# Optimization experiments

Measured on AMD Instinct MI355X. Metric: run time of the kernel, lower is better.

## Reference

```python
import jax, jax.numpy as jnp
import numpy as np

B, T, V = 32, 100, 20000
E, H, M, DD = 128, 128, 64, 2


def setup_inputs() -> dict:
    key = jax.random.key(0)
    ks = jax.random.split(key, 12)
    x = jax.random.uniform(ks[0], (B, T, V), dtype=jnp.float32)
    # zero out trailing timesteps per example so Masking layer matters
    lens = jax.random.randint(ks[1], (B,), T * 3 // 4, T + 1)
    tmask = (jnp.arange(T)[None, :] < lens[:, None]).astype(jnp.float32)
    x = x * tmask[:, :, None]
    a = jax.random.uniform(ks[2], (B, V), dtype=jnp.float32)
    d = jax.random.normal(ks[3], (B, DD), dtype=jnp.float32)
    # parameters
    emb = jax.random.uniform(ks[4], (V, E), minval=-0.1, maxval=0.1, dtype=jnp.float32)
    s = 1.0 / np.sqrt(E)
    gru_k = jax.random.uniform(ks[5], (E, 3 * H), minval=-s, maxval=s, dtype=jnp.float32)
    gru_rk = jax.random.normal(ks[6], (H, 3 * H), dtype=jnp.float32) / np.sqrt(H)
    gru_b_i = jnp.zeros((3 * H,), jnp.float32)   # input bias (reset_after=True)
    gru_b_r = jnp.zeros((3 * H,), jnp.float32)   # recurrent bias
    s1 = 1.0 / np.sqrt(H + E)
    W1 = jax.random.uniform(ks[7], (H + E, M), minval=-s1, maxval=s1, dtype=jnp.float32)
    b1 = jnp.zeros((M,), jnp.float32)
    s2 = 1.0 / np.sqrt(M + DD)
    W2 = jax.random.uniform(ks[8], (M + DD, 1), minval=-s2, maxval=s2, dtype=jnp.float32)
    b2 = jnp.zeros((1,), jnp.float32)
    return dict(x=x, a=a, d=d, emb=emb, gru_k=gru_k, gru_rk=gru_rk,
                gru_b_i=gru_b_i, gru_b_r=gru_b_r, W1=W1, b1=b1, W2=W2, b2=b2)


def _gru_final_state(xe, mask, gru_k, gru_rk, gru_b_i, gru_b_r):
    # xe: [B,T,E], mask: [B,T] bool. Keras GRU, reset_after=True, eval mode (dropout off).
    Hn = gru_rk.shape[0]
    x_proj = jnp.einsum('bte,eh->bth', xe, gru_k) + gru_b_i  # [B,T,3H]

    def step(h, inp):
        xp_t, m_t = inp                      # [B,3H], [B]
        rec = h @ gru_rk + gru_b_r           # [B,3H]
        xz, xr, xh = jnp.split(xp_t, 3, axis=-1)
        rz, rr, rh = jnp.split(rec, 3, axis=-1)
        z = jax.nn.sigmoid(xz + rz)
        r = jax.nn.sigmoid(xr + rr)
        hh = jnp.tanh(xh + r * rh)
        h_new = z * h + (1.0 - z) * hh
        h = jnp.where(m_t[:, None], h_new, h)  # masked steps carry state
        return h, None

    h0 = jnp.zeros((xe.shape[0], Hn), xe.dtype)
    h_final, _ = jax.lax.scan(step, h0, (jnp.swapaxes(x_proj, 0, 1), jnp.swapaxes(mask, 0, 1)))
    return h_final


def reference(x, a, d, emb, gru_k, gru_rk, gru_b_i, gru_b_r, W1, b1, W2, b2):
    ae = jnp.tanh(a @ emb)                       # [B,E]
    xe = jnp.tanh(jnp.einsum('btv,ve->bte', x, emb))  # [B,T,E]
    mask = jnp.any(xe != 0.0, axis=-1)           # Masking(mask_value=0.0)
    h = _gru_final_state(xe, mask, gru_k, gru_rk, gru_b_i, gru_b_r)  # [B,H]
    c = jnp.tanh(jnp.concatenate([h, ae], axis=1) @ W1 + b1)         # [B,M]
    out = jax.nn.sigmoid(jnp.concatenate([c, d], axis=1) @ W2 + b2)  # [B,1]
    return out
```

## Files before the change

kernel.cpp:

```cpp
#include <hip/hip_runtime.h>

typedef __attribute__((ext_vector_type(8))) short short8;
typedef __attribute__((ext_vector_type(4))) float float4v;

#define V_ 20000

__device__ __forceinline__ unsigned short f2bf(float f) {
    union { float f; unsigned int u; } v; v.f = f;
    unsigned int u = v.u;
    u += 0x7fffu + ((u >> 16) & 1u);
    return (unsigned short)(u >> 16);
}

__device__ __forceinline__ float fast_tanh(float x) {
    float xc = fminf(15.f, fmaxf(-15.f, x));
    float e = __expf(2.f * xc);
    return (e - 1.f) / (e + 1.f);
}

__device__ __forceinline__ float sigmoidf_(float x) {
    float xc = fminf(30.f, fmaxf(-30.f, x));
    return 1.f / (1.f + __expf(-xc));
}

#define GLL16(gp, lp) __builtin_amdgcn_global_load_lds( \
    (const __attribute__((address_space(1))) void*)(gp), \
    (__attribute__((address_space(3))) void*)(lp), 16, 0, 0)

__global__ __launch_bounds__(256) void cvt_embT(const float* __restrict__ emb,
                                                unsigned short* __restrict__ embT) {
    __shared__ unsigned short tile[128 * 65];
    int tid = threadIdx.x;
    int k0 = blockIdx.x * 64;
    const float4v* e4 = (const float4v*)emb;
    #pragma unroll
    for (int c = 0; c < 8; ++c) {
        int l4 = c * 256 + tid;
        int k = l4 >> 5;
        int n4 = l4 & 31;
        float4v f = {0.f, 0.f, 0.f, 0.f};
        if (k0 + k < V_) f = e4[(size_t)(k0 + k) * 32 + n4];
        tile[(n4 * 4 + 0) * 65 + k] = f2bf(f.x);
        tile[(n4 * 4 + 1) * 65 + k] = f2bf(f.y);
        tile[(n4 * 4 + 2) * 65 + k] = f2bf(f.z);
        tile[(n4 * 4 + 3) * 65 + k] = f2bf(f.w);
    }
    __syncthreads();
    #pragma unroll
    for (int c = 0; c < 4; ++c) {
        int l8 = c * 256 + tid;
        int n = l8 >> 3, seg = l8 & 7;
        int kk = k0 + seg * 8;
        if (kk < V_) {
            short8 v;
            #pragma unroll
            for (int i = 0; i < 8; ++i) v[i] = (short)tile[n * 65 + seg * 8 + i];
            *(short8*)(embT + (size_t)n * V_ + kk) = v;
        }
    }
}

__global__ __launch_bounds__(256, 4) void big_gemm(const float* __restrict__ x,
                                                   const float* __restrict__ a,
                                                   const unsigned short* __restrict__ embT,
                                                   float* __restrict__ partial,
                                                   int ks) {
    __shared__ unsigned short Alds[2][128 * 40];
    __shared__ unsigned short Blds[2][128 * 32];
    int tid = threadIdx.x;
    int bx = blockIdx.x, by = blockIdx.y;
    int m0 = bx * 128;
    int per = 625 / ks, extra = 625 % ks;
    int kb0 = by * per + (by < extra ? by : extra);
    int nkb = per + (by < extra ? 1 : 0);

    int lane = tid & 63, wave = tid >> 6;
    int wr = wave >> 1, wc = wave & 1;
    int ln = lane & 15, quad = lane >> 4;

    float4v acc[4][4];
    #pragma unroll
    for (int i = 0; i < 4; ++i)
        #pragma unroll
        for (int j = 0; j < 4; ++j) acc[i][j] = (float4v){0.f, 0.f, 0.f, 0.f};

    int row = tid >> 1, seg = tid & 1;
    int rg = m0 + row;
    int aidx = rg - 3200; aidx = aidx < 0 ? 0 : (aidx > 31 ? 31 : aidx);
    const float* __restrict__ srcA = (rg < 3200) ? (x + (size_t)rg * V_)
                                                 : (a + (size_t)aidx * V_);
    int brow0 = tid >> 2, bkq = tid & 3;
    int wbase = tid & ~63;
    const unsigned short* gB0 = embT + (size_t)brow0 * V_ + bkq * 8;
    const unsigned short* gB1 = embT + (size_t)(64 + brow0) * V_ + bkq * 8;

    float4v fa0, fa1, fa2, fa3;

    {
        int k0 = kb0 * 32;
        const float4v* ap = (const float4v*)(srcA + k0 + seg * 16);
        fa0 = ap[0]; fa1 = ap[1]; fa2 = ap[2]; fa3 = ap[3];
        GLL16(gB0 + k0, &Blds[0][(size_t)wbase * 8]);
        GLL16(gB1 + k0, &Blds[0][(size_t)(256 + wbase) * 8]);
        short8 w0, w1;
        w0[0]=(short)f2bf(fa0.x); w0[1]=(short)f2bf(fa0.y); w0[2]=(short)f2bf(fa0.z); w0[3]=(short)f2bf(fa0.w);
        w0[4]=(short)f2bf(fa1.x); w0[5]=(short)f2bf(fa1.y); w0[6]=(short)f2bf(fa1.z); w0[7]=(short)f2bf(fa1.w);
        w1[0]=(short)f2bf(fa2.x); w1[1]=(short)f2bf(fa2.y); w1[2]=(short)f2bf(fa2.z); w1[3]=(short)f2bf(fa2.w);
        w1[4]=(short)f2bf(fa3.x); w1[5]=(short)f2bf(fa3.y); w1[6]=(short)f2bf(fa3.z); w1[7]=(short)f2bf(fa3.w);
        *(short8*)&Alds[0][row * 40 + seg * 16]     = w0;
        *(short8*)&Alds[0][row * 40 + seg * 16 + 8] = w1;
    }
    __syncthreads();

    for (int it = 0; it < nkb; ++it) {
        int buf = it & 1, nxt = buf ^ 1;
        bool more = (it + 1 < nkb);
        if (more) {
            int k0 = (kb0 + it + 1) * 32;
            const float4v* ap = (const float4v*)(srcA + k0 + seg * 16);
            fa0 = ap[0]; fa1 = ap[1]; fa2 = ap[2]; fa3 = ap[3];
            GLL16(gB0 + k0, &Blds[nxt][(size_t)wbase * 8]);
            GLL16(gB1 + k0, &Blds[nxt][(size_t)(256 + wbase) * 8]);
        }
        short8 af[4];
        #pragma unroll
        for (int i = 0; i < 4; ++i)
            af[i] = *(const short8*)&Alds[buf][(wr * 64 + i * 16 + ln) * 40 + quad * 8];
        #pragma unroll
        for (int j = 0; j < 4; ++j) {
            short8 bf = *(const short8*)&Blds[buf][(wc * 64 + j * 16 + ln) * 32 + quad * 8];
            #pragma unroll
            for (int i = 0; i < 4; ++i)
                acc[i][j] = __builtin_amdgcn_mfma_f32_16x16x32_bf16(af[i], bf, acc[i][j], 0, 0, 0);
        }
        if (more) {
            short8 w0, w1;
            w0[0]=(short)f2bf(fa0.x); w0[1]=(short)f2bf(fa0.y); w0[2]=(short)f2bf(fa0.z); w0[3]=(short)f2bf(fa0.w);
            w0[4]=(short)f2bf(fa1.x); w0[5]=(short)f2bf(fa1.y); w0[6]=(short)f2bf(fa1.z); w0[7]=(short)f2bf(fa1.w);
            w1[0]=(short)f2bf(fa2.x); w1[1]=(short)f2bf(fa2.y); w1[2]=(short)f2bf(fa2.z); w1[3]=(short)f2bf(fa2.w);
            w1[4]=(short)f2bf(fa3.x); w1[5]=(short)f2bf(fa3.y); w1[6]=(short)f2bf(fa3.z); w1[7]=(short)f2bf(fa3.w);
            *(short8*)&Alds[nxt][row * 40 + seg * 16]     = w0;
            *(short8*)&Alds[nxt][row * 40 + seg * 16 + 8] = w1;
        }
        __syncthreads();
    }

    float* dst = partial + (size_t)by * 3328 * 128;
    #pragma unroll
    for (int i = 0; i < 4; ++i) {
        #pragma unroll
        for (int j = 0; j < 4; ++j) {
            int rowb = m0 + wr * 64 + i * 16 + quad * 4;
            int col = wc * 64 + j * 16 + ln;
            #pragma unroll
            for (int r = 0; r < 4; ++r)
                dst[(size_t)(rowb + r) * 128 + col] = acc[i][j][r];
        }
    }
}

__global__ __launch_bounds__(128) void reduce_tanh(const float* __restrict__ partial,
                                                   float* __restrict__ xe,
                                                   float* __restrict__ ae,
                                                   float* __restrict__ maskg,
                                                   int ks) {
    int row = blockIdx.x;
    int e = threadIdx.x;
    float s = 0.f;
    for (int k = 0; k < ks; ++k)
        s += partial[((size_t)k * 3328 + row) * 128 + e];
    float v = fast_tanh(s);
    if (row < 3200) {
        xe[(size_t)row * 128 + e] = v;
        __shared__ int any;
        if (e == 0) any = 0;
        __syncthreads();
        if (v != 0.f) any = 1;
        __syncthreads();
        if (e == 0) maskg[row] = any ? 1.f : 0.f;
    } else {
        ae[(row - 3200) * 128 + e] = v;
    }
}

__global__ __launch_bounds__(384) void xproj_kernel(const float* __restrict__ xe,
                                                    const float* __restrict__ gru_k,
                                                    const float* __restrict__ b_i,
                                                    float* __restrict__ xproj) {
    __shared__ float xs[16 * 128];
    int tid = threadIdx.x;
    int row0 = blockIdx.x * 16;
    const float4v* src = (const float4v*)(xe + (size_t)row0 * 128);
    float4v* dstl = (float4v*)xs;
    #pragma unroll
    for (int c = 0; c < 2; ++c) {
        int i4 = c * 384 + tid;
        if (i4 < 512) dstl[i4] = src[i4];
    }
    __syncthreads();
    int j = tid;
    float acc[16];
    #pragma unroll
    for (int r = 0; r < 16; ++r) acc[r] = 0.f;
    float bi = b_i[j];
    for (int k4 = 0; k4 < 32; ++k4) {
        float g0 = gru_k[(k4 * 4 + 0) * 384 + j];
        float g1 = gru_k[(k4 * 4 + 1) * 384 + j];
        float g2 = gru_k[(k4 * 4 + 2) * 384 + j];
        float g3 = gru_k[(k4 * 4 + 3) * 384 + j];
        #pragma unroll
        for (int r = 0; r < 16; ++r) {
            float4v xv = *(const float4v*)&xs[r * 128 + k4 * 4];
            acc[r] = fmaf(xv.x, g0, acc[r]);
            acc[r] = fmaf(xv.y, g1, acc[r]);
            acc[r] = fmaf(xv.z, g2, acc[r]);
            acc[r] = fmaf(xv.w, g3, acc[r]);
        }
    }
    #pragma unroll
    for (int r = 0; r < 16; ++r)
        xproj[(size_t)(row0 + r) * 384 + j] = acc[r] + bi;
}

__global__ __launch_bounds__(384) void gru_kernel(const float* __restrict__ xproj,
                                                  const float* __restrict__ maskg,
                                                  const float* __restrict__ gru_rk,
                                                  const float* __restrict__ b_r,
                                                  float* __restrict__ hout) {
    int b = blockIdx.x;
    int j = threadIdx.x;
    float w[128];
    #pragma unroll
    for (int k = 0; k < 128; ++k) w[k] = gru_rk[k * 384 + j];
    float br = b_r[j];
    __shared__ float4v hs4[32];
    __shared__ float recs[384];
    float* hs = (float*)hs4;
    float hreg = 0.f;
    if (j < 128) hs[j] = 0.f;
    const float* xp_base = xproj + (size_t)b * 100 * 384;
    const float* mk = maskg + b * 100;
    float xz = 0.f, xr = 0.f, xh = 0.f;
    if (j < 128) { xz = xp_base[j]; xr = xp_base[128 + j]; xh = xp_base[256 + j]; }
    __syncthreads();
    for (int t = 0; t < 100; ++t) {
        float nxz = 0.f, nxr = 0.f, nxh = 0.f;
        if (t < 99 && j < 128) {
            const float* nb = xp_base + (t + 1) * 384;
            nxz = nb[j]; nxr = nb[128 + j]; nxh = nb[256 + j];
        }
        float s0 = 0.f, s1 = 0.f, s2 = 0.f, s3 = 0.f;
        #pragma unroll
        for (int k4 = 0; k4 < 32; ++k4) {
            float4v hv = hs4[k4];
            s0 = fmaf(hv.x, w[k4 * 4 + 0], s0);
            s1 = fmaf(hv.y, w[k4 * 4 + 1], s1);
            s2 = fmaf(hv.z, w[k4 * 4 + 2], s2);
            s3 = fmaf(hv.w, w[k4 * 4 + 3], s3);
        }
        recs[j] = br + ((s0 + s1) + (s2 + s3));
        __syncthreads();
        if (j < 128) {
            float z = sigmoidf_(xz + recs[j]);
            float r = sigmoidf_(xr + recs[128 + j]);
            float hh = fast_tanh(xh + r * recs[256 + j]);
            float hn = z * hreg + (1.f - z) * hh;
            hreg = (mk[t] != 0.f) ? hn : hreg;
            hs[j] = hreg;
        }
        __syncthreads();
        xz = nxz; xr = nxr; xh = nxh;
    }
    if (j < 128) hout[b * 128 + j] = hreg;
}

__global__ __launch_bounds__(64) void head_kernel(const float* __restrict__ hout,
                                                  const float* __restrict__ ae,
                                                  const float* __restrict__ d,
                                                  const float* __restrict__ W1,
                                                  const float* __restrict__ b1,
                                                  const float* __restrict__ W2,
                                                  const float* __restrict__ b2,
                                                  float* __restrict__ out) {
    int b = blockIdx.x;
    int m = threadIdx.x;
    float s = b1[m];
    const float* hb = hout + b * 128;
    const float* ab = ae + b * 128;
    #pragma unroll 4
    for (int k = 0; k < 128; ++k) s = fmaf(hb[k], W1[k * 64 + m], s);
    #pragma unroll 4
    for (int k = 0; k < 128; ++k) s = fmaf(ab[k], W1[(128 + k) * 64 + m], s);
    float c = fast_tanh(s);
    float p = c * W2[m];
    #pragma unroll
    for (int off = 32; off > 0; off >>= 1) p += __shfl_down(p, off);
    if (m == 0) {
        p += d[b * 2 + 0] * W2[64] + d[b * 2 + 1] * W2[65] + b2[0];
        out[b] = sigmoidf_(p);
    }
}

extern "C" void kernel_launch(void* const* d_in, const int* in_sizes, int n_in,
                              void* d_out, int out_size, void* d_ws, size_t ws_size,
                              hipStream_t stream) {
    (void)in_sizes; (void)n_in; (void)out_size;
    const float* x      = (const float*)d_in[0];
    const float* a      = (const float*)d_in[1];
    const float* d      = (const float*)d_in[2];
    const float* emb    = (const float*)d_in[3];
    const float* gru_k  = (const float*)d_in[4];
    const float* gru_rk = (const float*)d_in[5];
    const float* gbi    = (const float*)d_in[6];
    const float* gbr    = (const float*)d_in[7];
    const float* W1     = (const float*)d_in[8];
    const float* b1     = (const float*)d_in[9];
    const float* W2     = (const float*)d_in[10];
    const float* b2     = (const float*)d_in[11];
    float* out = (float*)d_out;

    char* ws = (char*)d_ws;
    unsigned short* embT = (unsigned short*)(ws);
    float* xe      = (float*)(ws + 5120000);
    float* ae      = (float*)(ws + 6758400);
    float* maskg   = (float*)(ws + 6774784);
    float* xproj   = (float*)(ws + 6787584);
    float* hout    = (float*)(ws + 11702784);
    const size_t fixed = 11719168;
    const size_t slice = (size_t)3328 * 128 * 4;
    float* partial = (float*)(ws + fixed);

    int ks = 8;
    if (ws_size > fixed + slice) {
        size_t avail = (ws_size - fixed) / slice;
        ks = (int)(avail < 32 ? avail : 32);
        if (ks < 1) ks = 1;
    }

    hipLaunchKernelGGL(cvt_embT,    dim3(313),     dim3(256), 0, stream, emb, embT);
    hipLaunchKernelGGL(big_gemm,    dim3(26, ks),  dim3(256), 0, stream, x, a, embT, partial, ks);
    hipLaunchKernelGGL(reduce_tanh, dim3(3232),    dim3(128), 0, stream, partial, xe, ae, maskg, ks);
    hipLaunchKernelGGL(xproj_kernel,dim3(200),     dim3(384), 0, stream, xe, gru_k, gbi, xproj);
    hipLaunchKernelGGL(gru_kernel,  dim3(32),      dim3(384), 0, stream, xproj, maskg, gru_rk, gbr, hout);
    hipLaunchKernelGGL(head_kernel, dim3(32),      dim3(64),  0, stream, hout, ae, d, W1, b1, W2, b2, out);
}
```

Before: 573.5 us.

## Retile big GEMM to 16-row blocks streaming B directly from global

```diff
diff --git a/kernel.cpp b/kernel.cpp
--- a/kernel.cpp
+++ b/kernel.cpp
@@ -4,6 +4,8 @@
 typedef __attribute__((ext_vector_type(4))) float float4v;
 
 #define V_ 20000
+#define KS 8
+#define ARS 264
 
 __device__ __forceinline__ unsigned short f2bf(float f) {
     union { float f; unsigned int u; } v; v.f = f;
@@ -22,10 +24,6 @@
     float xc = fminf(30.f, fmaxf(-30.f, x));
     return 1.f / (1.f + __expf(-xc));
 }
-
-#define GLL16(gp, lp) __builtin_amdgcn_global_load_lds( \
-    (const __attribute__((address_space(1))) void*)(gp), \
-    (__attribute__((address_space(3))) void*)(lp), 16, 0, 0)
 
 __global__ __launch_bounds__(256) void cvt_embT(const float* __restrict__ emb,
                                                 unsigned short* __restrict__ embT) {
@@ -60,115 +58,119 @@
     }
 }
 
-__global__ __launch_bounds__(256, 4) void big_gemm(const float* __restrict__ x,
-                                                   const float* __restrict__ a,
-                                                   const unsigned short* __restrict__ embT,
-                                                   float* __restrict__ partial,
-                                                   int ks) {
-    __shared__ unsigned short Alds[2][128 * 40];
-    __shared__ unsigned short Blds[2][128 * 32];
+__global__ __launch_bounds__(256) void big_gemm(const float* __restrict__ x,
+                                                const float* __restrict__ a,
+                                                const unsigned short* __restrict__ embT,
+                                                float* __restrict__ partial) {
+    __shared__ unsigned short Alds[2][16 * ARS];
     int tid = threadIdx.x;
     int bx = blockIdx.x, by = blockIdx.y;
-    int m0 = bx * 128;
-    int per = 625 / ks, extra = 625 % ks;
-    int kb0 = by * per + (by < extra ? by : extra);
-    int nkb = per + (by < extra ? 1 : 0);
-
-    int lane = tid & 63, wave = tid >> 6;
-    int wr = wave >> 1, wc = wave & 1;
+    int m0 = bx * 16;
+    const int per = 79 / KS, extra = 79 % KS;
+    int sc0 = by * per + (by < extra ? by : extra);
+    int nsc = per + (by < extra ? 1 : 0);
+
+    int r = tid >> 4, c = tid & 15;
+    int rg = m0 + r;
+    const float* __restrict__ srcA = (rg < 3200) ? (x + (size_t)rg * V_)
+                                                 : (a + (size_t)(rg - 3200) * V_);
+    int lane = tid & 63, w = tid >> 6;
     int ln = lane & 15, quad = lane >> 4;
-
-    float4v acc[4][4];
-    #pragma unroll
-    for (int i = 0; i < 4; ++i)
-        #pragma unroll
-        for (int j = 0; j < 4; ++j) acc[i][j] = (float4v){0.f, 0.f, 0.f, 0.f};
-
-    int row = tid >> 1, seg = tid & 1;
-    int rg = m0 + row;
-    int aidx = rg - 3200; aidx = aidx < 0 ? 0 : (aidx > 31 ? 31 : aidx);
-    const float* __restrict__ srcA = (rg < 3200) ? (x + (size_t)rg * V_)
-                                                 : (a + (size_t)aidx * V_);
-    int brow0 = tid >> 2, bkq = tid & 3;
-    int wbase = tid & ~63;
-    const unsigned short* gB0 = embT + (size_t)brow0 * V_ + bkq * 8;
-    const unsigned short* gB1 = embT + (size_t)(64 + brow0) * V_ + bkq * 8;
-
-    float4v fa0, fa1, fa2, fa3;
+    const unsigned short* __restrict__ bb0 = embT + (size_t)(w * 32 + ln) * V_ + quad * 8;
+    const unsigned short* __restrict__ bb1 = bb0 + (size_t)16 * V_;
+    int aoff = ln * ARS + quad * 8;
+
+    float4v acc0 = {0.f, 0.f, 0.f, 0.f}, acc1 = {0.f, 0.f, 0.f, 0.f};
+    float4v p0, p1, p2, p3;
 
     {
-        int k0 = kb0 * 32;
-        const float4v* ap = (const float4v*)(srcA + k0 + seg * 16);
-        fa0 = ap[0]; fa1 = ap[1]; fa2 = ap[2]; fa3 = ap[3];
-        GLL16(gB0 + k0, &Blds[0][(size_t)wbase * 8]);
-        GLL16(gB1 + k0, &Blds[0][(size_t)(256 + wbase) * 8]);
+        int k0 = sc0 * 256;
+        int nkb = 625 - sc0 * 8; if (nkb > 8) nkb = 8;
+        int L = nkb * 32;
+        if (c * 16 < L) {
+            const float4v* ap = (const float4v*)(srcA + k0 + c * 16);
+            p0 = ap[0]; p1 = ap[1]; p2 = ap[2]; p3 = ap[3];
+        } else {
+            p0 = p1 = p2 = p3 = (float4v){0.f, 0.f, 0.f, 0.f};
+        }
         short8 w0, w1;
-        w0[0]=(short)f2bf(fa0.x); w0[1]=(short)f2bf(fa0.y); w0[2]=(short)f2bf(fa0.z); w0[3]=(short)f2bf(fa0.w);
-        w0[4]=(short)f2bf(fa1.x); w0[5]=(short)f2bf(fa1.y); w0[6]=(short)f2bf(fa1.z); w0[7]=(short)f2bf(fa1.w);
-        w1[0]=(short)f2bf(fa2.x); w1[1]=(short)f2bf(fa2.y); w1[2]=(short)f2bf(fa2.z); w1[3]=(short)f2bf(fa2.w);
-        w1[4]=(short)f2bf(fa3.x); w1[5]=(short)f2bf(fa3.y); w1[6]=(short)f2bf(fa3.z); w1[7]=(short)f2bf(fa3.w);
-        *(short8*)&Alds[0][row * 40 + seg * 16]     = w0;
-        *(short8*)&Alds[0][row * 40 + seg * 16 + 8] = w1;
+        w0[0]=(short)f2bf(p0.x); w0[1]=(short)f2bf(p0.y); w0[2]=(short)f2bf(p0.z); w0[3]=(short)f2bf(p0.w);
+        w0[4]=(short)f2bf(p1.x); w0[5]=(short)f2bf(p1.y); w0[6]=(short)f2bf(p1.z); w0[7]=(short)f2bf(p1.w);
+        w1[0]=(short)f2bf(p2.x); w1[1]=(short)f2bf(p2.y); w1[2]=(short)f2bf(p2.z); w1[3]=(short)f2bf(p2.w);
+        w1[4]=(short)f2bf(p3.x); w1[5]=(short)f2bf(p3.y); w1[6]=(short)f2bf(p3.z); w1[7]=(short)f2bf(p3.w);
+        *(short8*)&Alds[0][r * ARS + c * 16]     = w0;
+        *(short8*)&Alds[0][r * ARS + c * 16 + 8] = w1;
     }
     __syncthreads();
 
-    for (int it = 0; it < nkb; ++it) {
-        int buf = it & 1, nxt = buf ^ 1;
-        bool more = (it + 1 < nkb);
+    for (int s = 0; s < nsc; ++s) {
+        int buf = s & 1;
+        int sc = sc0 + s;
+        int k0 = sc * 256;
+        int nkb = 625 - sc * 8; if (nkb > 8) nkb = 8;
+        bool more = (s + 1 < nsc);
         if (more) {
-            int k0 = (kb0 + it + 1) * 32;
-            const float4v* ap = (const float4v*)(srcA + k0 + seg * 16);
-            fa0 = ap[0]; fa1 = ap[1]; fa2 = ap[2]; fa3 = ap[3];
-            GLL16(gB0 + k0, &Blds[nxt][(size_t)wbase * 8]);
-            GLL16(gB1 + k0, &Blds[nxt][(size_t)(256 + wbase) * 8]);
-        }
-        short8 af[4];
-        #pragma unroll
-        for (int i = 0; i < 4; ++i)
-            af[i] = *(const short8*)&Alds[buf][(wr * 64 + i * 16 + ln) * 40 + quad * 8];
-        #pragma unroll
-        for (int j = 0; j < 4; ++j) {
-            short8 bf = *(const short8*)&Blds[buf][(wc * 64 + j * 16 + ln) * 32 + quad * 8];
+            int k0n = (sc + 1) * 256;
+            int nkbn = 625 - (sc + 1) * 8; if (nkbn > 8) nkbn = 8;
+            if (c * 16 < nkbn * 32) {
+                const float4v* ap = (const float4v*)(srcA + k0n + c * 16);
+                p0 = ap[0]; p1 = ap[1]; p2 = ap[2]; p3 = ap[3];
+            } else {
+                p0 = p1 = p2 = p3 = (float4v){0.f, 0.f, 0.f, 0.f};
+            }
+        }
+        const unsigned short* bp0 = bb0 + k0;
+        const unsigned short* bp1 = bb1 + k0;
+        const unsigned short* al = &Alds[buf][aoff];
+        if (nkb == 8) {
             #pragma unroll
-            for (int i = 0; i < 4; ++i)
-                acc[i][j] = __builtin_amdgcn_mfma_f32_16x16x32_bf16(af[i], bf, acc[i][j], 0, 0, 0);
+            for (int kk = 0; kk < 8; ++kk) {
+                short8 af = *(const short8*)(al + kk * 32);
+                short8 f0 = *(const short8*)(bp0 + kk * 32);
+                short8 f1 = *(const short8*)(bp1 + kk * 32);
+                acc0 = __builtin_amdgcn_mfma_f32_16x16x32_bf16(af, f0, acc0, 0, 0, 0);
+                acc1 = __builtin_amdgcn_mfma_f32_16x16x32_bf16(af, f1, acc1, 0, 0, 0);
+            }
+        } else {
+            for (int kk = 0; kk < nkb; ++kk) {
+                short8 af = *(const short8*)(al + kk * 32);
+                short8 f0 = *(const short8*)(bp0 + kk * 32);
+                short8 f1 = *(const short8*)(bp1 + kk * 32);
+                acc0 = __builtin_amdgcn_mfma_f32_16x16x32_bf16(af, f0, acc0, 0, 0, 0);
+                acc1 = __builtin_amdgcn_mfma_f32_16x16x32_bf16(af, f1, acc1, 0, 0, 0);
+            }
         }
         if (more) {
+            int nxt = buf ^ 1;
             short8 w0, w1;
-            w0[0]=(short)f2bf(fa0.x); w0[1]=(short)f2bf(fa0.y); w0[2]=(short)f2bf(fa0.z); w0[3]=(short)f2bf(fa0.w);
-            w0[4]=(short)f2bf(fa1.x); w0[5]=(short)f2bf(fa1.y); w0[6]=(short)f2bf(fa1.z); w0[7]=(short)f2bf(fa1.w);
-            w1[0]=(short)f2bf(fa2.x); w1[1]=(short)f2bf(fa2.y); w1[2]=(short)f2bf(fa2.z); w1[3]=(short)f2bf(fa2.w);
-            w1[4]=(short)f2bf(fa3.x); w1[5]=(short)f2bf(fa3.y); w1[6]=(short)f2bf(fa3.z); w1[7]=(short)f2bf(fa3.w);
-            *(short8*)&Alds[nxt][row * 40 + seg * 16]     = w0;
-            *(short8*)&Alds[nxt][row * 40 + seg * 16 + 8] = w1;
-        }
-        __syncthreads();
-    }
-
-    float* dst = partial + (size_t)by * 3328 * 128;
-    #pragma unroll
-    for (int i = 0; i < 4; ++i) {
-        #pragma unroll
-        for (int j = 0; j < 4; ++j) {
-            int rowb = m0 + wr * 64 + i * 16 + quad * 4;
-            int col = wc * 64 + j * 16 + ln;
-            #pragma unroll
-            for (int r = 0; r < 4; ++r)
-                dst[(size_t)(rowb + r) * 128 + col] = acc[i][j][r];
-        }
+            w0[0]=(short)f2bf(p0.x); w0[1]=(short)f2bf(p0.y); w0[2]=(short)f2bf(p0.z); w0[3]=(short)f2bf(p0.w);
+            w0[4]=(short)f2bf(p1.x); w0[5]=(short)f2bf(p1.y); w0[6]=(short)f2bf(p1.z); w0[7]=(short)f2bf(p1.w);
+            w1[0]=(short)f2bf(p2.x); w1[1]=(short)f2bf(p2.y); w1[2]=(short)f2bf(p2.z); w1[3]=(short)f2bf(p2.w);
+            w1[4]=(short)f2bf(p3.x); w1[5]=(short)f2bf(p3.y); w1[6]=(short)f2bf(p3.z); w1[7]=(short)f2bf(p3.w);
+            *(short8*)&Alds[nxt][r * ARS + c * 16]     = w0;
+            *(short8*)&Alds[nxt][r * ARS + c * 16 + 8] = w1;
+        }
+        __syncthreads();
+    }
+
+    size_t base = ((size_t)by * 3232 + m0 + quad * 4) * 128 + w * 32 + ln;
+    #pragma unroll
+    for (int reg = 0; reg < 4; ++reg) {
+        partial[base + (size_t)reg * 128]      = acc0[reg];
+        partial[base + (size_t)reg * 128 + 16] = acc1[reg];
     }
 }
 
 __global__ __launch_bounds__(128) void reduce_tanh(const float* __restrict__ partial,
                                                    float* __restrict__ xe,
                                                    float* __restrict__ ae,
-                                                   float* __restrict__ maskg,
-                                                   int ks) {
+                                                   float* __restrict__ maskg) {
     int row = blockIdx.x;
     int e = threadIdx.x;
     float s = 0.f;
-    for (int k = 0; k < ks; ++k)
-        s += partial[((size_t)k * 3328 + row) * 128 + e];
+    #pragma unroll
+    for (int k = 0; k < KS; ++k)
+        s += partial[((size_t)k * 3232 + row) * 128 + e];
     float v = fast_tanh(s);
     if (row < 3200) {
         xe[(size_t)row * 128 + e] = v;
@@ -304,7 +306,7 @@
 extern "C" void kernel_launch(void* const* d_in, const int* in_sizes, int n_in,
                               void* d_out, int out_size, void* d_ws, size_t ws_size,
                               hipStream_t stream) {
-    (void)in_sizes; (void)n_in; (void)out_size;
+    (void)in_sizes; (void)n_in; (void)out_size; (void)ws_size;
     const float* x      = (const float*)d_in[0];
     const float* a      = (const float*)d_in[1];
     const float* d      = (const float*)d_in[2];
@@ -326,21 +328,12 @@
     float* maskg   = (float*)(ws + 6774784);
     float* xproj   = (float*)(ws + 6787584);
     float* hout    = (float*)(ws + 11702784);
-    const size_t fixed = 11719168;
-    const size_t slice = (size_t)3328 * 128 * 4;
-    float* partial = (float*)(ws + fixed);
-
-    int ks = 8;
-    if (ws_size > fixed + slice) {
-        size_t avail = (ws_size - fixed) / slice;
-        ks = (int)(avail < 32 ? avail : 32);
-        if (ks < 1) ks = 1;
-    }
-
-    hipLaunchKernelGGL(cvt_embT,    dim3(313),     dim3(256), 0, stream, emb, embT);
-    hipLaunchKernelGGL(big_gemm,    dim3(26, ks),  dim3(256), 0, stream, x, a, embT, partial, ks);
-    hipLaunchKernelGGL(reduce_tanh, dim3(3232),    dim3(128), 0, stream, partial, xe, ae, maskg, ks);
-    hipLaunchKernelGGL(xproj_kernel,dim3(200),     dim3(384), 0, stream, xe, gru_k, gbi, xproj);
-    hipLaunchKernelGGL(gru_kernel,  dim3(32),      dim3(384), 0, stream, xproj, maskg, gru_rk, gbr, hout);
-    hipLaunchKernelGGL(head_kernel, dim3(32),      dim3(64),  0, stream, hout, ae, d, W1, b1, W2, b2, out);
-}
+    float* partial = (float*)(ws + 11719168);
+
+    hipLaunchKernelGGL(cvt_embT,    dim3(313),      dim3(256), 0, stream, emb, embT);
+    hipLaunchKernelGGL(big_gemm,    dim3(202, KS),  dim3(256), 0, stream, x, a, embT, partial);
+    hipLaunchKernelGGL(reduce_tanh, dim3(3232),     dim3(128), 0, stream, partial, xe, ae, maskg);
+    hipLaunchKernelGGL(xproj_kernel,dim3(200),      dim3(384), 0, stream, xe, gru_k, gbi, xproj);
+    hipLaunchKernelGGL(gru_kernel,  dim3(32),       dim3(384), 0, stream, xproj, maskg, gru_rk, gbr, hout);
+    hipLaunchKernelGGL(head_kernel, dim3(32),       dim3(64),  0, stream, hout, ae, d, W1, b1, W2, b2, out);
+}
```

Result: slower. 601.3 us (+4.8%).
